# Performance work log

Measured on AMD Instinct MI355X. Metric: run time of the kernel, lower is better.

The kernel has to match this reference:

```python
import jax, jax.numpy as jnp
import numpy as np

NEG_SLOPE = 0.2   # negative_slope
EPS = 1e-6        # leaky-relu eps
BN_EPS = 1e-5     # torch BatchNorm default eps


def setup_inputs() -> dict:
    key = jax.random.key(0)
    k1, k2, k3 = jax.random.split(key, 3)
    B, C_in, C_out, N = 8, 256, 256, 8192
    x = jax.random.normal(k1, (B, C_in, 3, N), dtype=jnp.float32)
    s = 1.0 / np.sqrt(C_in)  # nn.Linear default init range
    W_feat = jax.random.uniform(k2, (C_out, C_in), minval=-s, maxval=s, dtype=jnp.float32)
    W_dir = jax.random.uniform(k3, (C_out, C_in), minval=-s, maxval=s, dtype=jnp.float32)
    gamma = jnp.ones((C_out,), jnp.float32)
    beta = jnp.zeros((C_out,), jnp.float32)
    return {"x": x, "W_feat": W_feat, "W_dir": W_dir, "gamma": gamma, "beta": beta}


def reference(x, W_feat, W_dir, gamma, beta):
    # VNLinear: kron(W, eye(3)) conv2d == per-vector channel mix
    p = jnp.einsum('oc,bcdn->bodn', W_feat, x)  # [B, O, 3, N]

    # VNBatchNorm: BN (training mode, batch stats) on vector norms, then rescale
    norm = jnp.sqrt(jnp.sum(p * p, axis=2))           # [B, O, N]
    mean = jnp.mean(norm, axis=(0, 2))                # [O]
    var = jnp.var(norm, axis=(0, 2))                  # [O] biased, as torch BN
    norm_bn = ((norm - mean[None, :, None]) * jax.lax.rsqrt(var + BN_EPS)[None, :, None]
               * gamma[None, :, None] + beta[None, :, None])
    p = p / norm[:, :, None, :] * norm_bn[:, :, None, :]

    # VNLeakyReLU with direction computed from the ORIGINAL input x
    d = jnp.einsum('oc,bcdn->bodn', W_dir, x)         # [B, O, 3, N]
    dot = jnp.sum(p * d, axis=2, keepdims=True)       # [B, O, 1, N]
    d_norm_sq = jnp.sum(d * d, axis=2, keepdims=True)
    return jnp.where(dot >= 0, p, p - (1.0 - NEG_SLOPE) * (dot / (d_norm_sq + EPS)) * d)
```

## Files before the change

### kernel.cpp

```cpp
#include <hip/hip_runtime.h>
#include <math.h>

#define BDIM 8
#define CIN  256
#define COUT 256
#define NDIM 8192

#define NEG_COEF  0.8f
#define LRELU_EPS 1e-6f
#define BN_EPS    1e-5f

typedef __attribute__((ext_vector_type(8))) short bf16x8;
typedef __attribute__((ext_vector_type(4))) float f32x4;

#define WS_WFH 0
#define WS_WFL 65536
#define WS_WDH 131072
#define WS_WDL 196608
#define WS_STATS_BYTE 524288
#define NSLOT 8
#define TILE_BYTES 12288
#define WS_XHI_BYTE 557056
#define XIMG_BYTES 100663296ull
#define WS_XLO_BYTE (WS_XHI_BYTE + XIMG_BYTES)
#define WS_NEED (WS_XLO_BYTE + XIMG_BYTES)

__device__ __forceinline__ unsigned short f2bf(float f) {
    unsigned u = __float_as_uint(f);
    return (unsigned short)((u + 0x7FFFu + ((u >> 16) & 1u)) >> 16);
}
__device__ __forceinline__ float bf2f(unsigned short h) {
    return __uint_as_float(((unsigned)h) << 16);
}

__device__ __forceinline__ int swz(int off) {
    return off ^ (((off >> 6) & 7) << 4);
}

__device__ __forceinline__ void gl_lds16(const char* g, char* l) {
    __builtin_amdgcn_global_load_lds(
        (const __attribute__((address_space(1))) unsigned int*)g,
        (__attribute__((address_space(3))) unsigned int*)l, 16, 0, 0);
}

__global__ __launch_bounds__(256) void setup_w_kernel(
    const float* __restrict__ Wf, const float* __restrict__ Wd,
    unsigned short* __restrict__ wsu)
{
    const int o = blockIdx.x;
    const int mat = blockIdx.y;
    const int c = threadIdx.x;
    const float* W = mat ? Wd : Wf;
    float w = W[o * CIN + c];
    unsigned short hi = f2bf(w);
    unsigned short lo = f2bf(w - bf2f(hi));
    int pos = (c & ~31) + 4 * (c & 7) + ((c >> 3) & 3);
    unsigned short* ph = wsu + (mat ? WS_WDH : WS_WFH);
    unsigned short* pl = wsu + (mat ? WS_WDL : WS_WFL);
    ph[o * CIN + pos] = hi;
    pl[o * CIN + pos] = lo;
}

__global__ __launch_bounds__(512) void vn_statscvt(
    const float* __restrict__ x, const unsigned short* __restrict__ wsu,
    char* __restrict__ xh, char* __restrict__ xl,
    float* __restrict__ stats)
{
    __shared__ uint4 sH4[TILE_BYTES / 16];
    __shared__ uint4 sL4[TILE_BYTES / 16];
    __shared__ float redS[256], redQ[256];
    char* sH = (char*)sH4;
    char* sL = (char*)sL4;

    const int t    = threadIdx.x;
    const int nblk = blockIdx.x;
    const int b    = blockIdx.z;
    const int n0   = nblk * 64;

    const int lane = t & 63;
    const int w    = t >> 6;
    const int q    = lane >> 4;
    const int ln   = lane & 15;

    const int jl = t & 31;
    const int kb = (t >> 5) & 7;
    const int u  = t >> 8;

    if (t < 256) { redS[t] = 0.f; redQ[t] = 0.f; }

    f32x4 acc[2][12];
    #pragma unroll
    for (int i = 0; i < 2; ++i)
        #pragma unroll
        for (int j = 0; j < 12; ++j) acc[i][j] = (f32x4)0.f;

    const unsigned short* wfh = wsu + WS_WFH;
    const int oo = w * 32;
    char* ghb = xh + ((size_t)(b * 128 + nblk)) * (8 * TILE_BYTES);
    char* glb = xl + ((size_t)(b * 128 + nblk)) * (8 * TILE_BYTES);

    for (int ct = 0; ct < 8; ++ct) {
        const int c0 = ct * 32;
        __syncthreads();
        #pragma unroll
        for (int s = 0; s < 3; ++s) {
            const int ip = u * 3 + s;
            const int jloc = ip * 32 + jl;
            const int d = jloc >> 6, nl = jloc & 63;
            float v[4];
            #pragma unroll
            for (int i = 0; i < 4; ++i) {
                int c = c0 + kb + 8 * i;
                v[i] = x[((size_t)((b * CIN + c) * 3 + d)) * NDIM + n0 + nl];
            }
            unsigned short h0 = f2bf(v[0]), h1 = f2bf(v[1]), h2 = f2bf(v[2]), h3 = f2bf(v[3]);
            uint2 ph = make_uint2((unsigned)h0 | ((unsigned)h1 << 16),
                                  (unsigned)h2 | ((unsigned)h3 << 16));
            uint2 pl = make_uint2(
                (unsigned)f2bf(v[0] - bf2f(h0)) | ((unsigned)f2bf(v[1] - bf2f(h1)) << 16),
                (unsigned)f2bf(v[2] - bf2f(h2)) | ((unsigned)f2bf(v[3] - bf2f(h3)) << 16));
            const int off = swz(jloc * 64 + kb * 8);
            *(uint2*)(sH + off) = ph;
            *(uint2*)(sL + off) = pl;
        }
        __syncthreads();
        {
            const int off = t * 48;
            const char* src = (off < TILE_BYTES) ? (sH + off) : (sL + off - TILE_BYTES);
            char* dst = (off < TILE_BYTES) ? (ghb + ct * TILE_BYTES + off)
                                           : (glb + ct * TILE_BYTES + off - TILE_BYTES);
            #pragma unroll
            for (int p = 0; p < 3; ++p)
                *(uint4*)(dst + p * 16) = *(const uint4*)(src + p * 16);
        }
        bf16x8 af[2];
        #pragma unroll
        for (int mt = 0; mt < 2; ++mt)
            af[mt] = *(const bf16x8*)&wfh[(oo + mt * 16 + ln) * CIN + c0 + q * 8];
        #pragma unroll
        for (int nt = 0; nt < 12; ++nt) {
            const int jloc = nt * 16 + ln;
            bf16x8 bh = *(const bf16x8*)(sH + swz(jloc * 64 + q * 16));
            #pragma unroll
            for (int mt = 0; mt < 2; ++mt)
                acc[mt][nt] = __builtin_amdgcn_mfma_f32_16x16x32_bf16(af[mt], bh, acc[mt][nt], 0, 0, 0);
        }
    }

    #pragma unroll
    for (int mt = 0; mt < 2; ++mt) {
        #pragma unroll
        for (int r = 0; r < 4; ++r) {
            float s = 0.f, s2 = 0.f;
            #pragma unroll
            for (int h = 0; h < 4; ++h) {
                float p0 = acc[mt][0 + h][r];
                float p1 = acc[mt][4 + h][r];
                float p2 = acc[mt][8 + h][r];
                float n2 = p0 * p0 + p1 * p1 + p2 * p2;
                s += sqrtf(n2); s2 += n2;
            }
            #pragma unroll
            for (int m = 1; m < 16; m <<= 1) {
                s  += __shfl_xor(s,  m, 64);
                s2 += __shfl_xor(s2, m, 64);
            }
            if (ln == 0) {
                int o = oo + mt * 16 + q * 4 + r;
                atomicAdd(&redS[o], s);
                atomicAdd(&redQ[o], s2);
            }
        }
    }
    __syncthreads();
    if (t < 256) {
        int slot = nblk & (NSLOT - 1);
        atomicAdd(&stats[slot * 256 + t], redS[t]);
        atomicAdd(&stats[NSLOT * 256 + slot * 256 + t], redQ[t]);
    }
}

__global__ __launch_bounds__(256) void vn_finalize2(
    float* __restrict__ stats, const float* __restrict__ gamma)
{
    int o = threadIdx.x;
    float s = 0.f, s2 = 0.f;
    #pragma unroll
    for (int i = 0; i < NSLOT; ++i) {
        s  += stats[i * 256 + o];
        s2 += stats[(NSLOT + i) * 256 + o];
    }
    const float inv = 1.0f / (float)(BDIM * NDIM);
    float mean = s * inv;
    float var  = fmaxf(s2 * inv - mean * mean, 0.f);
    stats[2 * NSLOT * 256 + o] = mean;
    stats[2 * NSLOT * 256 + 256 + o] = gamma[o] * rsqrtf(var + BN_EPS);
}

__global__ __launch_bounds__(256) void vn_main2(
    const unsigned short* __restrict__ wsu,
    const char* __restrict__ xh, const char* __restrict__ xl,
    const float* __restrict__ stats, const float* __restrict__ beta,
    float* __restrict__ out)
{
    __shared__ uint4 sH4[TILE_BYTES / 16];
    __shared__ uint4 sL4[TILE_BYTES / 16];
    char* sH = (char*)sH4;
    char* sL = (char*)sL4;

    const int t    = threadIdx.x;
    const int nblk = blockIdx.x;
    const int n0   = nblk * 64;
    const int o0   = blockIdx.y * 64;
    const int b    = blockIdx.z;

    const int lane = t & 63;
    const int w    = t >> 6;
    const int q    = lane >> 4;
    const int ln   = lane & 15;

    f32x4 accP[2][6], accD[2][6];
    #pragma unroll
    for (int i = 0; i < 2; ++i)
        #pragma unroll
        for (int j = 0; j < 6; ++j) { accP[i][j] = (f32x4)0.f; accD[i][j] = (f32x4)0.f; }

    const unsigned short* wfh = wsu + WS_WFH;
    const unsigned short* wfl = wsu + WS_WFL;
    const unsigned short* wdh = wsu + WS_WDH;
    const unsigned short* wdl = wsu + WS_WDL;
    const int oo = o0 + (w >> 1) * 32;
    const int nb = (w & 1) * 32;

    const char* ghb = xh + ((size_t)(b * 128 + nblk)) * (8 * TILE_BYTES);
    const char* glb = xl + ((size_t)(b * 128 + nblk)) * (8 * TILE_BYTES);

    for (int ct = 0; ct < 8; ++ct) {
        __syncthreads();
        #pragma unroll
        for (int p = 0; p < 3; ++p) {
            gl_lds16(ghb + ct * TILE_BYTES + t * 16 + p * 4096, sH + t * 16 + p * 4096);
            gl_lds16(glb + ct * TILE_BYTES + t * 16 + p * 4096, sL + t * 16 + p * 4096);
        }
        __syncthreads();

        const int c0 = ct * 32;
        bf16x8 afh[2], afl[2], adh[2], adl[2];
        #pragma unroll
        for (int mt = 0; mt < 2; ++mt) {
            const int row = (oo + mt * 16 + ln) * CIN + c0 + q * 8;
            afh[mt] = *(const bf16x8*)&wfh[row];
            afl[mt] = *(const bf16x8*)&wfl[row];
            adh[mt] = *(const bf16x8*)&wdh[row];
            adl[mt] = *(const bf16x8*)&wdl[row];
        }
        #pragma unroll
        for (int nt = 0; nt < 6; ++nt) {
            const int d = nt >> 1, h = nt & 1;
            const int jloc = d * 64 + nb + h * 16 + ln;
            const int off = swz(jloc * 64 + q * 16);
            bf16x8 bh = *(const bf16x8*)(sH + off);
            bf16x8 bl = *(const bf16x8*)(sL + off);
            #pragma unroll
            for (int mt = 0; mt < 2; ++mt) {
                f32x4 aP = accP[mt][nt];
                aP = __builtin_amdgcn_mfma_f32_16x16x32_bf16(afh[mt], bh, aP, 0, 0, 0);
                aP = __builtin_amdgcn_mfma_f32_16x16x32_bf16(afh[mt], bl, aP, 0, 0, 0);
                aP = __builtin_amdgcn_mfma_f32_16x16x32_bf16(afl[mt], bh, aP, 0, 0, 0);
                aP = __builtin_amdgcn_mfma_f32_16x16x32_bf16(afl[mt], bl, aP, 0, 0, 0);
                accP[mt][nt] = aP;
                f32x4 aD = accD[mt][nt];
                aD = __builtin_amdgcn_mfma_f32_16x16x32_bf16(adh[mt], bh, aD, 0, 0, 0);
                aD = __builtin_amdgcn_mfma_f32_16x16x32_bf16(adh[mt], bl, aD, 0, 0, 0);
                aD = __builtin_amdgcn_mfma_f32_16x16x32_bf16(adl[mt], bh, aD, 0, 0, 0);
                accD[mt][nt] = aD;
            }
        }
    }

    const float* meanp  = stats + 2 * NSLOT * 256;
    const float* scalep = meanp + 256;
    #pragma unroll
    for (int mt = 0; mt < 2; ++mt) {
        #pragma unroll
        for (int r = 0; r < 4; ++r) {
            const int o = oo + mt * 16 + q * 4 + r;
            const float mean  = meanp[o];
            const float scale = scalep[o];
            const float bet   = beta[o];
            #pragma unroll
            for (int h = 0; h < 2; ++h) {
                float p0 = accP[mt][0 + h][r], p1 = accP[mt][2 + h][r], p2 = accP[mt][4 + h][r];
                float d0 = accD[mt][0 + h][r], d1 = accD[mt][2 + h][r], d2 = accD[mt][4 + h][r];
                float n2 = p0 * p0 + p1 * p1 + p2 * p2;
                float nr = sqrtf(n2);
                float f  = ((nr - mean) * scale + bet) / nr;
                p0 *= f; p1 *= f; p2 *= f;
                float dot = p0 * d0 + p1 * d1 + p2 * d2;
                if (dot < 0.f) {
                    float g = NEG_COEF * dot / (d0 * d0 + d1 * d1 + d2 * d2 + LRELU_EPS);
                    p0 -= g * d0; p1 -= g * d1; p2 -= g * d2;
                }
                const int n = n0 + nb + h * 16 + ln;
                out[((size_t)(b * COUT + o) * 3 + 0) * NDIM + n] = p0;
                out[((size_t)(b * COUT + o) * 3 + 1) * NDIM + n] = p1;
                out[((size_t)(b * COUT + o) * 3 + 2) * NDIM + n] = p2;
            }
        }
    }
}

__global__ __launch_bounds__(256) void vn_stats_mfma(
    const float* __restrict__ x, const unsigned short* __restrict__ wsu,
    float* __restrict__ stats)
{
    __shared__ unsigned short sXhi[192 * 40];
    __shared__ float redS[64], redQ[64];

    const int t  = threadIdx.x;
    const int n0 = blockIdx.x * 64;
    const int o0 = blockIdx.y * 64;
    const int b  = blockIdx.z;

    const int lane = t & 63;
    const int w    = t >> 6;
    const int q    = lane >> 4;
    const int ln   = lane & 15;

    const int jl = t & 31;
    const int kb = t >> 5;

    if (t < 64) { redS[t] = 0.f; redQ[t] = 0.f; }

    f32x4 acc[2][6];
    #pragma unroll
    for (int i = 0; i < 2; ++i)
        #pragma unroll
        for (int j = 0; j < 6; ++j) acc[i][j] = (f32x4)0.f;

    const unsigned short* wfh = wsu + WS_WFH;
    const int oo = o0 + (w >> 1) * 32;
    const int nb = (w & 1) * 32;

    for (int c0 = 0; c0 < CIN; c0 += 32) {
        __syncthreads();
        #pragma unroll
        for (int ip = 0; ip < 6; ++ip) {
            int jloc = ip * 32 + jl;
            int d = jloc >> 6, nl = jloc & 63;
            float v[4];
            #pragma unroll
            for (int i = 0; i < 4; ++i) {
                int c = c0 + kb + 8 * i;
                v[i] = x[((size_t)((b * CIN + c) * 3 + d)) * NDIM + n0 + nl];
            }
            unsigned p0 = (unsigned)f2bf(v[0]) | ((unsigned)f2bf(v[1]) << 16);
            unsigned p1 = (unsigned)f2bf(v[2]) | ((unsigned)f2bf(v[3]) << 16);
            *(uint2*)&sXhi[jloc * 40 + kb * 4] = make_uint2(p0, p1);
        }
        __syncthreads();
        bf16x8 af[2];
        #pragma unroll
        for (int mt = 0; mt < 2; ++mt)
            af[mt] = *(const bf16x8*)&wfh[(oo + mt * 16 + ln) * CIN + c0 + q * 8];
        #pragma unroll
        for (int nt = 0; nt < 6; ++nt) {
            int d = nt >> 1, h = nt & 1;
            int jloc = d * 64 + nb + h * 16 + ln;
            bf16x8 bh = *(const bf16x8*)&sXhi[jloc * 40 + q * 8];
            #pragma unroll
            for (int mt = 0; mt < 2; ++mt)
                acc[mt][nt] = __builtin_amdgcn_mfma_f32_16x16x32_bf16(af[mt], bh, acc[mt][nt], 0, 0, 0);
        }
    }

    #pragma unroll
    for (int mt = 0; mt < 2; ++mt) {
        #pragma unroll
        for (int r = 0; r < 4; ++r) {
            float s = 0.f, s2 = 0.f;
            #pragma unroll
            for (int h = 0; h < 2; ++h) {
                float p0 = acc[mt][0 + h][r];
                float p1 = acc[mt][2 + h][r];
                float p2 = acc[mt][4 + h][r];
                float n2 = p0 * p0 + p1 * p1 + p2 * p2;
                s += sqrtf(n2); s2 += n2;
            }
            #pragma unroll
            for (int m = 1; m < 16; m <<= 1) {
                s  += __shfl_xor(s,  m, 64);
                s2 += __shfl_xor(s2, m, 64);
            }
            if (ln == 0) {
                int ol = (w >> 1) * 32 + mt * 16 + q * 4 + r;
                atomicAdd(&redS[ol], s);
                atomicAdd(&redQ[ol], s2);
            }
        }
    }
    __syncthreads();
    if (t < 64) {
        int slot = blockIdx.x & (NSLOT - 1);
        atomicAdd(&stats[slot * 256 + o0 + t], redS[t]);
        atomicAdd(&stats[NSLOT * 256 + slot * 256 + o0 + t], redQ[t]);
    }
}

__global__ __launch_bounds__(256) void vn_main_mfma(
    const float* __restrict__ x, const unsigned short* __restrict__ wsu,
    const float* __restrict__ stats, const float* __restrict__ beta,
    float* __restrict__ out)
{
    __shared__ unsigned short sXhi[192 * 40];
    __shared__ unsigned short sXlo[192 * 40];

    const int t  = threadIdx.x;
    const int n0 = blockIdx.x * 64;
    const int o0 = blockIdx.y * 64;
    const int b  = blockIdx.z;

    const int lane = t & 63;
    const int w    = t >> 6;
    const int q    = lane >> 4;
    const int ln   = lane & 15;

    const int jl = t & 31;
    const int kb = t >> 5;

    f32x4 accP[2][6], accD[2][6];
    #pragma unroll
    for (int i = 0; i < 2; ++i)
        #pragma unroll
        for (int j = 0; j < 6; ++j) { accP[i][j] = (f32x4)0.f; accD[i][j] = (f32x4)0.f; }

    const unsigned short* wfh = wsu + WS_WFH;
    const unsigned short* wfl = wsu + WS_WFL;
    const unsigned short* wdh = wsu + WS_WDH;
    const unsigned short* wdl = wsu + WS_WDL;
    const int oo = o0 + (w >> 1) * 32;
    const int nb = (w & 1) * 32;

    for (int c0 = 0; c0 < CIN; c0 += 32) {
        __syncthreads();
        #pragma unroll
        for (int ip = 0; ip < 6; ++ip) {
            int jloc = ip * 32 + jl;
            int d = jloc >> 6, nl = jloc & 63;
            float v[4];
            #pragma unroll
            for (int i = 0; i < 4; ++i) {
                int c = c0 + kb + 8 * i;
                v[i] = x[((size_t)((b * CIN + c) * 3 + d)) * NDIM + n0 + nl];
            }
            unsigned short h0 = f2bf(v[0]), h1 = f2bf(v[1]), h2 = f2bf(v[2]), h3 = f2bf(v[3]);
            unsigned ph0 = (unsigned)h0 | ((unsigned)h1 << 16);
            unsigned ph1 = (unsigned)h2 | ((unsigned)h3 << 16);
            unsigned pl0 = (unsigned)f2bf(v[0] - bf2f(h0)) | ((unsigned)f2bf(v[1] - bf2f(h1)) << 16);
            unsigned pl1 = (unsigned)f2bf(v[2] - bf2f(h2)) | ((unsigned)f2bf(v[3] - bf2f(h3)) << 16);
            *(uint2*)&sXhi[jloc * 40 + kb * 4] = make_uint2(ph0, ph1);
            *(uint2*)&sXlo[jloc * 40 + kb * 4] = make_uint2(pl0, pl1);
        }
        __syncthreads();
        bf16x8 afh[2], afl[2], adh[2], adl[2];
        #pragma unroll
        for (int mt = 0; mt < 2; ++mt) {
            int row = (oo + mt * 16 + ln) * CIN + c0 + q * 8;
            afh[mt] = *(const bf16x8*)&wfh[row];
            afl[mt] = *(const bf16x8*)&wfl[row];
            adh[mt] = *(const bf16x8*)&wdh[row];
            adl[mt] = *(const bf16x8*)&wdl[row];
        }
        #pragma unroll
        for (int nt = 0; nt < 6; ++nt) {
            int d = nt >> 1, h = nt & 1;
            int jloc = d * 64 + nb + h * 16 + ln;
            bf16x8 bh = *(const bf16x8*)&sXhi[jloc * 40 + q * 8];
            bf16x8 bl = *(const bf16x8*)&sXlo[jloc * 40 + q * 8];
            #pragma unroll
            for (int mt = 0; mt < 2; ++mt) {
                f32x4 aP = accP[mt][nt];
                aP = __builtin_amdgcn_mfma_f32_16x16x32_bf16(afh[mt], bh, aP, 0, 0, 0);
                aP = __builtin_amdgcn_mfma_f32_16x16x32_bf16(afh[mt], bl, aP, 0, 0, 0);
                aP = __builtin_amdgcn_mfma_f32_16x16x32_bf16(afl[mt], bh, aP, 0, 0, 0);
                aP = __builtin_amdgcn_mfma_f32_16x16x32_bf16(afl[mt], bl, aP, 0, 0, 0);
                accP[mt][nt] = aP;
                f32x4 aD = accD[mt][nt];
                aD = __builtin_amdgcn_mfma_f32_16x16x32_bf16(adh[mt], bh, aD, 0, 0, 0);
                aD = __builtin_amdgcn_mfma_f32_16x16x32_bf16(adh[mt], bl, aD, 0, 0, 0);
                aD = __builtin_amdgcn_mfma_f32_16x16x32_bf16(adl[mt], bh, aD, 0, 0, 0);
                accD[mt][nt] = aD;
            }
        }
    }

    const float* meanp  = stats + 2 * NSLOT * 256;
    const float* scalep = meanp + 256;
    #pragma unroll
    for (int mt = 0; mt < 2; ++mt) {
        #pragma unroll
        for (int r = 0; r < 4; ++r) {
            const int o = oo + mt * 16 + q * 4 + r;
            const float mean  = meanp[o];
            const float scale = scalep[o];
            const float bet   = beta[o];
            #pragma unroll
            for (int h = 0; h < 2; ++h) {
                float p0 = accP[mt][0 + h][r], p1 = accP[mt][2 + h][r], p2 = accP[mt][4 + h][r];
                float d0 = accD[mt][0 + h][r], d1 = accD[mt][2 + h][r], d2 = accD[mt][4 + h][r];
                float n2 = p0 * p0 + p1 * p1 + p2 * p2;
                float nr = sqrtf(n2);
                float f  = ((nr - mean) * scale + bet) / nr;
                p0 *= f; p1 *= f; p2 *= f;
                float dot = p0 * d0 + p1 * d1 + p2 * d2;
                if (dot < 0.f) {
                    float g = NEG_COEF * dot / (d0 * d0 + d1 * d1 + d2 * d2 + LRELU_EPS);
                    p0 -= g * d0; p1 -= g * d1; p2 -= g * d2;
                }
                const int n = n0 + nb + h * 16 + ln;
                out[((size_t)(b * COUT + o) * 3 + 0) * NDIM + n] = p0;
                out[((size_t)(b * COUT + o) * 3 + 1) * NDIM + n] = p1;
                out[((size_t)(b * COUT + o) * 3 + 2) * NDIM + n] = p2;
            }
        }
    }
}

extern "C" void kernel_launch(void* const* d_in, const int* in_sizes, int n_in,
                              void* d_out, int out_size, void* d_ws, size_t ws_size,
                              hipStream_t stream) {
    const float* x     = (const float*)d_in[0];
    const float* Wf    = (const float*)d_in[1];
    const float* Wd    = (const float*)d_in[2];
    const float* gamma = (const float*)d_in[3];
    const float* beta  = (const float*)d_in[4];
    float* out = (float*)d_out;
    unsigned short* wsu = (unsigned short*)d_ws;
    float* stats = (float*)((char*)d_ws + WS_STATS_BYTE);

    hipMemsetAsync((char*)d_ws + WS_STATS_BYTE, 0, 2 * NSLOT * 256 * sizeof(float), stream);
    setup_w_kernel<<<dim3(256, 2), 256, 0, stream>>>(Wf, Wd, wsu);

    if (ws_size >= (size_t)WS_NEED) {
        char* xhp = (char*)d_ws + WS_XHI_BYTE;
        char* xlp = (char*)d_ws + WS_XLO_BYTE;
        vn_statscvt<<<dim3(128, 1, 8), 512, 0, stream>>>(x, wsu, xhp, xlp, stats);
        vn_finalize2<<<1, 256, 0, stream>>>(stats, gamma);
        vn_main2<<<dim3(128, 4, 8), 256, 0, stream>>>(wsu, xhp, xlp, stats, beta, out);
    } else {
        dim3 grid(NDIM / 64, COUT / 64, BDIM);
        vn_stats_mfma<<<grid, 256, 0, stream>>>(x, wsu, stats);
        vn_finalize2<<<1, 256, 0, stream>>>(stats, gamma);
        vn_main_mfma<<<grid, 256, 0, stream>>>(x, wsu, stats, beta, out);
    }
}
```

Baseline: 708.4 us.

## Split convert from stats and double-buffer LDS tiles in stats and main kernels

The fused stats+convert kernel becomes two kernels. A standalone convert kernel with a wide grid writes the swizzled hi/lo bf16 images of x directly to global memory. A stats kernel then reads only the hi image, split over two output-channel halves. Both the stats and main GEMM kernels now double-buffer LDS tiles, prefetching the next channel tile while running MFMAs on the current one, which removes one barrier per iteration. The cost is an extra kernel launch, a re-read of the hi image, and twice the LDS per block in the main kernel, which may lower occupancy.

Result: faster. 632.2 us (-10.7%).

```diff
diff --git a/kernel.cpp b/kernel.cpp
--- a/kernel.cpp
+++ b/kernel.cpp
@@ -61,32 +61,101 @@
     pl[o * CIN + pos] = lo;
 }
 
-__global__ __launch_bounds__(512) void vn_statscvt(
-    const float* __restrict__ x, const unsigned short* __restrict__ wsu,
-    char* __restrict__ xh, char* __restrict__ xl,
-    float* __restrict__ stats)
-{
-    __shared__ uint4 sH4[TILE_BYTES / 16];
-    __shared__ uint4 sL4[TILE_BYTES / 16];
-    __shared__ float redS[256], redQ[256];
-    char* sH = (char*)sH4;
-    char* sL = (char*)sL4;
-
+__global__ __launch_bounds__(256) void vn_convert(
+    const float* __restrict__ x,
+    char* __restrict__ xh, char* __restrict__ xl)
+{
     const int t    = threadIdx.x;
     const int nblk = blockIdx.x;
+    const int ct   = blockIdx.y;
     const int b    = blockIdx.z;
     const int n0   = nblk * 64;
+    const int c0   = ct * 32;
+
+    char* gh = xh + ((size_t)(b * 128 + nblk)) * (8 * TILE_BYTES) + ct * TILE_BYTES;
+    char* gl = xl + ((size_t)(b * 128 + nblk)) * (8 * TILE_BYTES) + ct * TILE_BYTES;
+
+    #pragma unroll
+    for (int p = 0; p < 3; ++p) {
+        const int m  = p * 256 + t;
+        const int dr = m >> 2, dp = m & 3;
+        const int sr = (dr & ~1) | ((dr ^ (dr >> 2)) & 1);
+        const int sp = dp ^ (sr & 3);
+        const int d  = sr >> 6, nl = sr & 63;
+        const int kb = sp * 2;
+        float v[8];
+        #pragma unroll
+        for (int i = 0; i < 4; ++i) {
+            const float* base = x + ((size_t)((b * CIN + c0 + kb + 8 * i) * 3 + d)) * NDIM + n0 + nl;
+            v[i]     = base[0];
+            v[4 + i] = base[3 * NDIM];
+        }
+        unsigned short h[8];
+        #pragma unroll
+        for (int j = 0; j < 8; ++j) h[j] = f2bf(v[j]);
+        uint4 H = make_uint4((unsigned)h[0] | ((unsigned)h[1] << 16),
+                             (unsigned)h[2] | ((unsigned)h[3] << 16),
+                             (unsigned)h[4] | ((unsigned)h[5] << 16),
+                             (unsigned)h[6] | ((unsigned)h[7] << 16));
+        unsigned short lo[8];
+        #pragma unroll
+        for (int j = 0; j < 8; ++j) lo[j] = f2bf(v[j] - bf2f(h[j]));
+        uint4 L = make_uint4((unsigned)lo[0] | ((unsigned)lo[1] << 16),
+                             (unsigned)lo[2] | ((unsigned)lo[3] << 16),
+                             (unsigned)lo[4] | ((unsigned)lo[5] << 16),
+                             (unsigned)lo[6] | ((unsigned)lo[7] << 16));
+        *(uint4*)(gh + m * 16) = H;
+        *(uint4*)(gl + m * 16) = L;
+    }
+}
+
+__device__ __forceinline__ void stats_step(
+    int ct, const char* gh, const char* srd, char* swr,
+    int t, int q, int ln, int oo,
+    const unsigned short* wfh, f32x4 (*acc)[12])
+{
+    if (ct < 7) {
+        #pragma unroll
+        for (int p = 0; p < 3; ++p)
+            gl_lds16(gh + (ct + 1) * TILE_BYTES + t * 16 + p * 4096,
+                     swr + t * 16 + p * 4096);
+    }
+    bf16x8 af[2];
+    #pragma unroll
+    for (int mt = 0; mt < 2; ++mt)
+        af[mt] = *(const bf16x8*)&wfh[(oo + mt * 16 + ln) * CIN + ct * 32 + q * 8];
+    #pragma unroll
+    for (int nt = 0; nt < 12; ++nt) {
+        bf16x8 bh = *(const bf16x8*)(srd + swz((nt * 16 + ln) * 64 + q * 16));
+        #pragma unroll
+        for (int mt = 0; mt < 2; ++mt)
+            acc[mt][nt] = __builtin_amdgcn_mfma_f32_16x16x32_bf16(af[mt], bh, acc[mt][nt], 0, 0, 0);
+    }
+    __syncthreads();
+}
+
+__global__ __launch_bounds__(256) void vn_stats2(
+    const unsigned short* __restrict__ wsu, const char* __restrict__ xh,
+    float* __restrict__ stats)
+{
+    __shared__ uint4 sA4[TILE_BYTES / 16];
+    __shared__ uint4 sB4[TILE_BYTES / 16];
+    __shared__ float redS[128], redQ[128];
+    char* sA = (char*)sA4;
+    char* sB = (char*)sB4;
+
+    const int t    = threadIdx.x;
+    const int nblk = blockIdx.x;
+    const int oy   = blockIdx.y;
+    const int b    = blockIdx.z;
 
     const int lane = t & 63;
     const int w    = t >> 6;
     const int q    = lane >> 4;
     const int ln   = lane & 15;
-
-    const int jl = t & 31;
-    const int kb = (t >> 5) & 7;
-    const int u  = t >> 8;
-
-    if (t < 256) { redS[t] = 0.f; redQ[t] = 0.f; }
+    const int oo   = oy * 128 + w * 32;
+
+    if (t < 128) { redS[t] = 0.f; redQ[t] = 0.f; }
 
     f32x4 acc[2][12];
     #pragma unroll
@@ -95,56 +164,16 @@
         for (int j = 0; j < 12; ++j) acc[i][j] = (f32x4)0.f;
 
     const unsigned short* wfh = wsu + WS_WFH;
-    const int oo = w * 32;
-    char* ghb = xh + ((size_t)(b * 128 + nblk)) * (8 * TILE_BYTES);
-    char* glb = xl + ((size_t)(b * 128 + nblk)) * (8 * TILE_BYTES);
-
-    for (int ct = 0; ct < 8; ++ct) {
-        const int c0 = ct * 32;
-        __syncthreads();
-        #pragma unroll
-        for (int s = 0; s < 3; ++s) {
-            const int ip = u * 3 + s;
-            const int jloc = ip * 32 + jl;
-            const int d = jloc >> 6, nl = jloc & 63;
-            float v[4];
-            #pragma unroll
-            for (int i = 0; i < 4; ++i) {
-                int c = c0 + kb + 8 * i;
-                v[i] = x[((size_t)((b * CIN + c) * 3 + d)) * NDIM + n0 + nl];
-            }
-            unsigned short h0 = f2bf(v[0]), h1 = f2bf(v[1]), h2 = f2bf(v[2]), h3 = f2bf(v[3]);
-            uint2 ph = make_uint2((unsigned)h0 | ((unsigned)h1 << 16),
-                                  (unsigned)h2 | ((unsigned)h3 << 16));
-            uint2 pl = make_uint2(
-                (unsigned)f2bf(v[0] - bf2f(h0)) | ((unsigned)f2bf(v[1] - bf2f(h1)) << 16),
-                (unsigned)f2bf(v[2] - bf2f(h2)) | ((unsigned)f2bf(v[3] - bf2f(h3)) << 16));
-            const int off = swz(jloc * 64 + kb * 8);
-            *(uint2*)(sH + off) = ph;
-            *(uint2*)(sL + off) = pl;
-        }
-        __syncthreads();
-        {
-            const int off = t * 48;
-            const char* src = (off < TILE_BYTES) ? (sH + off) : (sL + off - TILE_BYTES);
-            char* dst = (off < TILE_BYTES) ? (ghb + ct * TILE_BYTES + off)
-                                           : (glb + ct * TILE_BYTES + off - TILE_BYTES);
-            #pragma unroll
-            for (int p = 0; p < 3; ++p)
-                *(uint4*)(dst + p * 16) = *(const uint4*)(src + p * 16);
-        }
-        bf16x8 af[2];
-        #pragma unroll
-        for (int mt = 0; mt < 2; ++mt)
-            af[mt] = *(const bf16x8*)&wfh[(oo + mt * 16 + ln) * CIN + c0 + q * 8];
-        #pragma unroll
-        for (int nt = 0; nt < 12; ++nt) {
-            const int jloc = nt * 16 + ln;
-            bf16x8 bh = *(const bf16x8*)(sH + swz(jloc * 64 + q * 16));
-            #pragma unroll
-            for (int mt = 0; mt < 2; ++mt)
-                acc[mt][nt] = __builtin_amdgcn_mfma_f32_16x16x32_bf16(af[mt], bh, acc[mt][nt], 0, 0, 0);
-        }
+    const char* gh = xh + ((size_t)(b * 128 + nblk)) * (8 * TILE_BYTES);
+
+    #pragma unroll
+    for (int p = 0; p < 3; ++p)
+        gl_lds16(gh + t * 16 + p * 4096, sA + t * 16 + p * 4096);
+    __syncthreads();
+
+    for (int cp = 0; cp < 4; ++cp) {
+        stats_step(2 * cp,     gh, sA, sB, t, q, ln, oo, wfh, acc);
+        stats_step(2 * cp + 1, gh, sB, sA, t, q, ln, oo, wfh, acc);
     }
 
     #pragma unroll
@@ -166,17 +195,17 @@
                 s2 += __shfl_xor(s2, m, 64);
             }
             if (ln == 0) {
-                int o = oo + mt * 16 + q * 4 + r;
-                atomicAdd(&redS[o], s);
-                atomicAdd(&redQ[o], s2);
+                int ol = w * 32 + mt * 16 + q * 4 + r;
+                atomicAdd(&redS[ol], s);
+                atomicAdd(&redQ[ol], s2);
             }
         }
     }
     __syncthreads();
-    if (t < 256) {
+    if (t < 128) {
         int slot = nblk & (NSLOT - 1);
-        atomicAdd(&stats[slot * 256 + t], redS[t]);
-        atomicAdd(&stats[NSLOT * 256 + slot * 256 + t], redQ[t]);
+        atomicAdd(&stats[slot * 256 + oy * 128 + t], redS[t]);
+        atomicAdd(&stats[NSLOT * 256 + slot * 256 + oy * 128 + t], redQ[t]);
     }
 }
 
@@ -197,16 +226,72 @@
     stats[2 * NSLOT * 256 + 256 + o] = gamma[o] * rsqrtf(var + BN_EPS);
 }
 
-__global__ __launch_bounds__(256) void vn_main2(
+__device__ __forceinline__ void main_step(
+    int ct, const char* ghb, const char* glb,
+    const char* shr, const char* slr, char* shw, char* slw,
+    int t, int q, int ln, int oo, int nb,
+    const unsigned short* wfh, const unsigned short* wfl,
+    const unsigned short* wdh, const unsigned short* wdl,
+    f32x4 (*accP)[6], f32x4 (*accD)[6])
+{
+    if (ct < 7) {
+        #pragma unroll
+        for (int p = 0; p < 3; ++p) {
+            gl_lds16(ghb + (ct + 1) * TILE_BYTES + t * 16 + p * 4096,
+                     shw + t * 16 + p * 4096);
+            gl_lds16(glb + (ct + 1) * TILE_BYTES + t * 16 + p * 4096,
+                     slw + t * 16 + p * 4096);
+        }
+    }
+    const int c0 = ct * 32;
+    bf16x8 afh[2], afl[2], adh[2], adl[2];
+    #pragma unroll
+    for (int mt = 0; mt < 2; ++mt) {
+        const int row = (oo + mt * 16 + ln) * CIN + c0 + q * 8;
+        afh[mt] = *(const bf16x8*)&wfh[row];
+        afl[mt] = *(const bf16x8*)&wfl[row];
+        adh[mt] = *(const bf16x8*)&wdh[row];
+        adl[mt] = *(const bf16x8*)&wdl[row];
+    }
+    #pragma unroll
+    for (int nt = 0; nt < 6; ++nt) {
+        const int d = nt >> 1, h = nt & 1;
+        const int jloc = d * 64 + nb + h * 16 + ln;
+        const int off = swz(jloc * 64 + q * 16);
+        bf16x8 bh = *(const bf16x8*)(shr + off);
+        bf16x8 bl = *(const bf16x8*)(slr + off);
+        #pragma unroll
+        for (int mt = 0; mt < 2; ++mt) {
+            f32x4 aP = accP[mt][nt];
+            aP = __builtin_amdgcn_mfma_f32_16x16x32_bf16(afh[mt], bh, aP, 0, 0, 0);
+            aP = __builtin_amdgcn_mfma_f32_16x16x32_bf16(afh[mt], bl, aP, 0, 0, 0);
+            aP = __builtin_amdgcn_mfma_f32_16x16x32_bf16(afl[mt], bh, aP, 0, 0, 0);
+            aP = __builtin_amdgcn_mfma_f32_16x16x32_bf16(afl[mt], bl, aP, 0, 0, 0);
+            accP[mt][nt] = aP;
+            f32x4 aD = accD[mt][nt];
+            aD = __builtin_amdgcn_mfma_f32_16x16x32_bf16(adh[mt], bh, aD, 0, 0, 0);
+            aD = __builtin_amdgcn_mfma_f32_16x16x32_bf16(adh[mt], bl, aD, 0, 0, 0);
+            aD = __builtin_amdgcn_mfma_f32_16x16x32_bf16(adl[mt], bh, aD, 0, 0, 0);
+            accD[mt][nt] = aD;
+        }
+    }
+    __syncthreads();
+}
+
+__global__ __launch_bounds__(256) void vn_main3(
     const unsigned short* __restrict__ wsu,
     const char* __restrict__ xh, const char* __restrict__ xl,
     const float* __restrict__ stats, const float* __restrict__ beta,
     float* __restrict__ out)
 {
-    __shared__ uint4 sH4[TILE_BYTES / 16];
-    __shared__ uint4 sL4[TILE_BYTES / 16];
-    char* sH = (char*)sH4;
-    char* sL = (char*)sL4;
+    __shared__ uint4 sHA4[TILE_BYTES / 16];
+    __shared__ uint4 sHB4[TILE_BYTES / 16];
+    __shared__ uint4 sLA4[TILE_BYTES / 16];
+    __shared__ uint4 sLB4[TILE_BYTES / 16];
+    char* sHA = (char*)sHA4;
+    char* sHB = (char*)sHB4;
+    char* sLA = (char*)sLA4;
+    char* sLB = (char*)sLB4;
 
     const int t    = threadIdx.x;
     const int nblk = blockIdx.x;
@@ -235,47 +320,18 @@
     const char* ghb = xh + ((size_t)(b * 128 + nblk)) * (8 * TILE_BYTES);
     const char* glb = xl + ((size_t)(b * 128 + nblk)) * (8 * TILE_BYTES);
 
-    for (int ct = 0; ct < 8; ++ct) {
-        __syncthreads();
-        #pragma unroll
-        for (int p = 0; p < 3; ++p) {
-            gl_lds16(ghb + ct * TILE_BYTES + t * 16 + p * 4096, sH + t * 16 + p * 4096);
-            gl_lds16(glb + ct * TILE_BYTES + t * 16 + p * 4096, sL + t * 16 + p * 4096);
-        }
-        __syncthreads();
-
-        const int c0 = ct * 32;
-        bf16x8 afh[2], afl[2], adh[2], adl[2];
-        #pragma unroll
-        for (int mt = 0; mt < 2; ++mt) {
-            const int row = (oo + mt * 16 + ln) * CIN + c0 + q * 8;
-            afh[mt] = *(const bf16x8*)&wfh[row];
-            afl[mt] = *(const bf16x8*)&wfl[row];
-            adh[mt] = *(const bf16x8*)&wdh[row];
-            adl[mt] = *(const bf16x8*)&wdl[row];
-        }
-        #pragma unroll
-        for (int nt = 0; nt < 6; ++nt) {
-            const int d = nt >> 1, h = nt & 1;
-            const int jloc = d * 64 + nb + h * 16 + ln;
-            const int off = swz(jloc * 64 + q * 16);
-            bf16x8 bh = *(const bf16x8*)(sH + off);
-            bf16x8 bl = *(const bf16x8*)(sL + off);
-            #pragma unroll
-            for (int mt = 0; mt < 2; ++mt) {
-                f32x4 aP = accP[mt][nt];
-                aP = __builtin_amdgcn_mfma_f32_16x16x32_bf16(afh[mt], bh, aP, 0, 0, 0);
-                aP = __builtin_amdgcn_mfma_f32_16x16x32_bf16(afh[mt], bl, aP, 0, 0, 0);
-                aP = __builtin_amdgcn_mfma_f32_16x16x32_bf16(afl[mt], bh, aP, 0, 0, 0);
-                aP = __builtin_amdgcn_mfma_f32_16x16x32_bf16(afl[mt], bl, aP, 0, 0, 0);
-                accP[mt][nt] = aP;
-                f32x4 aD = accD[mt][nt];
-                aD = __builtin_amdgcn_mfma_f32_16x16x32_bf16(adh[mt], bh, aD, 0, 0, 0);
-                aD = __builtin_amdgcn_mfma_f32_16x16x32_bf16(adh[mt], bl, aD, 0, 0, 0);
-                aD = __builtin_amdgcn_mfma_f32_16x16x32_bf16(adl[mt], bh, aD, 0, 0, 0);
-                accD[mt][nt] = aD;
-            }
-        }
+    #pragma unroll
+    for (int p = 0; p < 3; ++p) {
+        gl_lds16(ghb + t * 16 + p * 4096, sHA + t * 16 + p * 4096);
+        gl_lds16(glb + t * 16 + p * 4096, sLA + t * 16 + p * 4096);
+    }
+    __syncthreads();
+
+    for (int cp = 0; cp < 4; ++cp) {
+        main_step(2 * cp,     ghb, glb, sHA, sLA, sHB, sLB,
+                  t, q, ln, oo, nb, wfh, wfl, wdh, wdl, accP, accD);
+        main_step(2 * cp + 1, ghb, glb, sHB, sLB, sHA, sLA,
+                  t, q, ln, oo, nb, wfh, wfl, wdh, wdl, accP, accD);
     }
 
     const float* meanp  = stats + 2 * NSLOT * 256;
@@ -544,9 +600,10 @@
     if (ws_size >= (size_t)WS_NEED) {
         char* xhp = (char*)d_ws + WS_XHI_BYTE;
         char* xlp = (char*)d_ws + WS_XLO_BYTE;
-        vn_statscvt<<<dim3(128, 1, 8), 512, 0, stream>>>(x, wsu, xhp, xlp, stats);
+        vn_convert<<<dim3(128, 8, 8), 256, 0, stream>>>(x, xhp, xlp);
+        vn_stats2<<<dim3(128, 2, 8), 256, 0, stream>>>(wsu, xhp, stats);
         vn_finalize2<<<1, 256, 0, stream>>>(stats, gamma);
-        vn_main2<<<dim3(128, 4, 8), 256, 0, stream>>>(wsu, xhp, xlp, stats, beta, out);
+        vn_main3<<<dim3(128, 4, 8), 256, 0, stream>>>(wsu, xhp, xlp, stats, beta, out);
     } else {
         dim3 grid(NDIM / 64, COUT / 64, BDIM);
         vn_stats_mfma<<<grid, 256, 0, stream>>>(x, wsu, stats);
```
